# Kernel tuning notes

Hardware: AMD Instinct MI355X
Metric: run time of the kernel (lower is better)

Reference implementation:

```python
import jax, jax.numpy as jnp
import numpy as np

EPS = 1e-5
N_HEAD = 16

def _ln(x, g, b):
    m = jnp.mean(x, -1, keepdims=True)
    v = jnp.mean((x - m) ** 2, -1, keepdims=True)
    return (x - m) * jax.lax.rsqrt(v + EPS) * g + b

def _mlp(x, fc_w, fc_b, proj_w, proj_b):
    h = x @ fc_w.T + fc_b
    h = h * jax.nn.sigmoid(1.702 * h)  # QuickGELU
    return h @ proj_w.T + proj_b

def setup_inputs() -> dict:
    key = jax.random.key(0)
    ks = jax.random.split(key, 16)
    S, B, D, BOX = 577, 8, 1024, 16
    sc = 0.02
    return {
        'x': jax.random.normal(ks[0], (S, B, D), jnp.float32),
        'detection_attn_mask': jax.random.normal(ks[1], (B * BOX * N_HEAD, 1, S), jnp.float32),
        'box_coords': jax.random.uniform(ks[2], (B, BOX, 4), jnp.float32),
        'layers': 24,
        'need_patch': 0,
        'in_proj_w': sc * jax.random.normal(ks[3], (3 * D, D), jnp.float32),
        'in_proj_b': jnp.zeros((3 * D,), jnp.float32),
        'out_w': sc * jax.random.normal(ks[4], (D, D), jnp.float32),
        'out_b': jnp.zeros((D,), jnp.float32),
        'ln1_g': jnp.ones((D,), jnp.float32),
        'ln1_b': jnp.zeros((D,), jnp.float32),
        'ln2_g': jnp.ones((D,), jnp.float32),
        'ln2_b': jnp.zeros((D,), jnp.float32),
        'fc_w': sc * jax.random.normal(ks[5], (4 * D, D), jnp.float32),
        'fc_b': jnp.zeros((4 * D,), jnp.float32),
        'proj_w': sc * jax.random.normal(ks[6], (D, 4 * D), jnp.float32),
        'proj_b': jnp.zeros((D,), jnp.float32),
    }

def reference(x, detection_attn_mask, box_coords, layers, need_patch,
              in_proj_w, in_proj_b, out_w, out_b,
              ln1_g, ln1_b, ln2_g, ln2_b, fc_w, fc_b, proj_w, proj_b):
    # step == layers-1, detection_attn_mask is not None, need_patch is False.
    S, B, D = x.shape
    H = N_HEAD
    hd = D // H
    BOX = box_coords.shape[1]  # uniform boxes per image

    h = _ln(x, ln1_g, ln1_b)                       # [S,B,D]
    qkv = h @ in_proj_w.T + in_proj_b              # [S,B,3D]
    q, k, v = jnp.split(qkv, 3, axis=-1)

    # query is sliced to the CLS token only (q[:, :1, :] after head split)
    q0 = q[0].reshape(B, H, hd) / jnp.sqrt(jnp.asarray(hd, x.dtype))  # [B,H,hd]
    kh = k.reshape(S, B, H, hd).transpose(1, 2, 0, 3)                 # [B,H,S,hd]
    vh = v.reshape(S, B, H, hd).transpose(1, 2, 0, 3)                 # [B,H,S,hd]

    attn = jnp.einsum('bhe,bhse->bhs', q0, kh)     # [B,H,S]

    # mask rows are ordered (batch, box, head); Nt == 1 is squeezed
    mask = detection_attn_mask.reshape(B, BOX, H, S)
    p_exp = jax.nn.softmax(attn[:, None] + mask, axis=-1)             # [B,BOX,H,S]
    out_exp = jnp.einsum('bxhs,bhse->bxhe', p_exp, vh).reshape(B * BOX, D)
    out_exp = out_exp @ out_w.T + out_b            # [B*BOX, D]

    p = jax.nn.softmax(attn, axis=-1)
    out = jnp.einsum('bhs,bhse->bhe', p, vh).reshape(B, D) @ out_w.T + out_b

    cls = x[0] + out                               # residual with CLS token
    cls = cls + _mlp(_ln(cls, ln2_g, ln2_b), fc_w, fc_b, proj_w, proj_b)

    x0_exp = jnp.repeat(x[0], BOX, axis=0)         # [B*BOX, D], batch-major
    mask_cls = x0_exp + out_exp
    mask_cls = mask_cls + _mlp(_ln(mask_cls, ln2_g, ln2_b), fc_w, fc_b, proj_w, proj_b)

    return mask_cls[None], cls[None]               # [1,B*BOX,D], [1,B,D]
```

## Files before the change

### kernel.cpp

```cpp
#include <hip/hip_runtime.h>
#include <stdint.h>

typedef unsigned short u16;
typedef unsigned int u32;
typedef __bf16 bf16x8 __attribute__((ext_vector_type(8)));
typedef float f32x4 __attribute__((ext_vector_type(4)));

__device__ __forceinline__ float bf2f(u16 u) {
  u32 v = ((u32)u) << 16;
  return __builtin_bit_cast(float, v);
}
__device__ __forceinline__ u16 f2bf(float f) {
  u32 u = __builtin_bit_cast(u32, f);
  u32 r = u + 0x7fffu + ((u >> 16) & 1u);
  return (u16)(r >> 16);
}

__device__ __forceinline__ float block_sum4(float v, float* red, int t) {
#pragma unroll
  for (int o = 32; o; o >>= 1) v += __shfl_xor(v, o, 64);
  if ((t & 63) == 0) red[t >> 6] = v;
  __syncthreads();
  float r = red[0] + red[1] + red[2] + red[3];
  __syncthreads();
  return r;
}

#define GLD16(gp, lp)                                                   \
  __builtin_amdgcn_global_load_lds(                                     \
      (const __attribute__((address_space(1))) void*)(gp),              \
      (__attribute__((address_space(3))) void*)(lp), 16, 0, 0)

__global__ __launch_bounds__(256) void cvt_f32_bf16(
    const float* __restrict__ S, u16* __restrict__ D, int n) {
  int i = (blockIdx.x * 256 + threadIdx.x) * 4;
  if (i < n) {
    float4 f = *(const float4*)(S + i);
    u32 lo = (u32)f2bf(f.x) | ((u32)f2bf(f.y) << 16);
    u32 hi = (u32)f2bf(f.z) | ((u32)f2bf(f.w) << 16);
    uint2 val = {lo, hi};
    *(uint2*)(D + i) = val;
  }
}

__global__ __launch_bounds__(256) void ln_rows_f32(
    const float* __restrict__ X, const float* __restrict__ G,
    const float* __restrict__ Bt, u16* __restrict__ O) {
  __shared__ float red[4];
  int row = blockIdx.x, t = threadIdx.x;
  float4 xv = *(const float4*)(X + (size_t)row * 1024 + t * 4);
  float v[4] = {xv.x, xv.y, xv.z, xv.w};
  float s = v[0] + v[1] + v[2] + v[3];
  s = block_sum4(s, red, t);
  float mean = s * (1.f / 1024.f);
  float q = 0.f;
#pragma unroll
  for (int i = 0; i < 4; ++i) { float d = v[i] - mean; q += d * d; }
  q = block_sum4(q, red, t);
  float rstd = rsqrtf(q * (1.f / 1024.f) + 1e-5f);
  float4 g = *(const float4*)(G + t * 4);
  float4 b = *(const float4*)(Bt + t * 4);
  float gg[4] = {g.x, g.y, g.z, g.w}, bb[4] = {b.x, b.y, b.z, b.w};
  u16 o[4];
#pragma unroll
  for (int i = 0; i < 4; ++i) o[i] = f2bf((v[i] - mean) * rstd * gg[i] + bb[i]);
  u32* op = (u32*)(O + (size_t)row * 1024 + t * 4);
  op[0] = (u32)o[0] | ((u32)o[1] << 16);
  op[1] = (u32)o[2] | ((u32)o[3] << 16);
}

__global__ __launch_bounds__(256) void resid_ln_f32(
    const float* __restrict__ X, const float* __restrict__ P,
    const float* __restrict__ G, const float* __restrict__ Bt,
    float* __restrict__ CLS, u16* __restrict__ H2) {
  __shared__ float red[4];
  int row = blockIdx.x, t = threadIdx.x;
  int bi = (row < 128) ? (row >> 4) : (row - 128);
  float4 xv = *(const float4*)(X + (size_t)bi * 1024 + t * 4);
  float4 pv = *(const float4*)(P + (size_t)row * 1024 + t * 4);
  float v[4] = {xv.x + pv.x, xv.y + pv.y, xv.z + pv.z, xv.w + pv.w};
  float* cp = CLS + (size_t)row * 1024 + t * 4;
#pragma unroll
  for (int i = 0; i < 4; ++i) cp[i] = v[i];
  float s = v[0] + v[1] + v[2] + v[3];
  s = block_sum4(s, red, t);
  float mean = s * (1.f / 1024.f);
  float q = 0.f;
#pragma unroll
  for (int i = 0; i < 4; ++i) { float d = v[i] - mean; q += d * d; }
  q = block_sum4(q, red, t);
  float rstd = rsqrtf(q * (1.f / 1024.f) + 1e-5f);
  float4 g = *(const float4*)(G + t * 4);
  float4 b = *(const float4*)(Bt + t * 4);
  float gg[4] = {g.x, g.y, g.z, g.w}, bb[4] = {b.x, b.y, b.z, b.w};
  u16 o[4];
#pragma unroll
  for (int i = 0; i < 4; ++i) o[i] = f2bf((v[i] - mean) * rstd * gg[i] + bb[i]);
  u32* op = (u32*)(H2 + (size_t)row * 1024 + t * 4);
  op[0] = (u32)o[0] | ((u32)o[1] << 16);
  op[1] = (u32)o[2] | ((u32)o[3] << 16);
}

__global__ __launch_bounds__(256) void gemm_bt_128(
    const u16* __restrict__ A, int lda, const u16* __restrict__ W, int ldw,
    const float* __restrict__ bias, u16* __restrict__ C, int ldc,
    int M, int N, int K) {
  __shared__ u16 As[128 * 64];
  __shared__ u16 Bs[128 * 64];
  int t = threadIdx.x, lane = t & 63, wv = t >> 6;
  int bm = blockIdx.x * 128, bn = blockIdx.y * 128;
  int quad = lane >> 4, rlow = lane & 15;
  int lrow = lane >> 3, lcol = (lane & 7) * 8;
  int wrow = (wv & 1) * 64, wcol = (wv >> 1) * 64;
  f32x4 acc[4][4] = {};

  for (int k0 = 0; k0 < K; k0 += 64) {
    __syncthreads();
#pragma unroll
    for (int j = 0; j < 4; ++j) {
      int rb = j * 4 + wv;
      int row = rb * 8 + lrow;
      int gm = bm + row; if (gm >= M) gm = M - 1;
      GLD16(A + (size_t)gm * lda + k0 + lcol, &As[rb * 8 * 64]);
      int gn = bn + row; if (gn >= N) gn = N - 1;
      GLD16(W + (size_t)gn * ldw + k0 + lcol, &Bs[rb * 8 * 64]);
    }
    __syncthreads();
#pragma unroll
    for (int kk = 0; kk < 64; kk += 32) {
      bf16x8 a[4], b[4];
#pragma unroll
      for (int i = 0; i < 4; ++i)
        a[i] = *(const bf16x8*)(&As[(wrow + i * 16 + rlow) * 64 + kk + quad * 8]);
#pragma unroll
      for (int j = 0; j < 4; ++j)
        b[j] = *(const bf16x8*)(&Bs[(wcol + j * 16 + rlow) * 64 + kk + quad * 8]);
#pragma unroll
      for (int i = 0; i < 4; ++i)
#pragma unroll
        for (int j = 0; j < 4; ++j)
          acc[i][j] = __builtin_amdgcn_mfma_f32_16x16x32_bf16(a[i], b[j], acc[i][j], 0, 0, 0);
    }
  }
#pragma unroll
  for (int j = 0; j < 4; ++j) {
    int gn = bn + wcol + j * 16 + rlow;
    float bv = (gn < N) ? bias[gn] : 0.f;
#pragma unroll
    for (int i = 0; i < 4; ++i)
#pragma unroll
      for (int r = 0; r < 4; ++r) {
        int gm = bm + wrow + i * 16 + quad * 4 + r;
        if (gm < M && gn < N) C[(size_t)gm * ldc + gn] = f2bf(acc[i][j][r] + bv);
      }
  }
}

#define LDT 72
__global__ __launch_bounds__(256) void gemm_bt_splitk(
    const u16* __restrict__ A, int lda, const u16* __restrict__ W, int ldw,
    float* __restrict__ ACC, int ldc, int M, int N, int KC) {
  __shared__ u16 As[64 * LDT];
  __shared__ u16 Bs[64 * LDT];
  int t = threadIdx.x;
  int bm = blockIdx.x * 64, bn = blockIdx.y * 64;
  int kbase = blockIdx.z * KC;
  int lane = t & 63, wv = t >> 6;
  f32x4 acc[4] = {};
  int srow = t >> 3;
  int scol = (t & 7) * 8;

  for (int k0 = kbase; k0 < kbase + KC; k0 += 64) {
    __syncthreads();
#pragma unroll
    for (int rr = 0; rr < 2; ++rr) {
      int r = srow + rr * 32;
      int gm = bm + r;
      uint4 da = {0, 0, 0, 0};
      if (gm < M) da = *(const uint4*)(A + (size_t)gm * lda + k0 + scol);
      *(uint4*)(&As[r * LDT + scol]) = da;
      int gn = bn + r;
      uint4 dw = {0, 0, 0, 0};
      if (gn < N) dw = *(const uint4*)(W + (size_t)gn * ldw + k0 + scol);
      *(uint4*)(&Bs[r * LDT + scol]) = dw;
    }
    __syncthreads();
    int quad = lane >> 4, rlow = lane & 15;
#pragma unroll
    for (int kk = 0; kk < 64; kk += 32) {
      bf16x8 a = *(const bf16x8*)(&As[(wv * 16 + rlow) * LDT + kk + quad * 8]);
#pragma unroll
      for (int j = 0; j < 4; ++j) {
        bf16x8 b = *(const bf16x8*)(&Bs[(j * 16 + rlow) * LDT + kk + quad * 8]);
        acc[j] = __builtin_amdgcn_mfma_f32_16x16x32_bf16(a, b, acc[j], 0, 0, 0);
      }
    }
  }
  int quad = lane >> 4, cidx = lane & 15;
#pragma unroll
  for (int j = 0; j < 4; ++j) {
    int gn = bn + j * 16 + cidx;
#pragma unroll
    for (int r = 0; r < 4; ++r) {
      int gm = bm + wv * 16 + quad * 4 + r;
      if (gm < M && gn < N) atomicAdd(&ACC[(size_t)gm * ldc + gn], acc[j][r]);
    }
  }
}

__global__ __launch_bounds__(256) void acc_init(
    float* __restrict__ ACC, const float* __restrict__ bias, int nmask, int total) {
  int i = (blockIdx.x * 256 + threadIdx.x) * 4;
  if (i < total) {
#pragma unroll
    for (int k = 0; k < 4; ++k) ACC[i + k] = bias[(i + k) & nmask];
  }
}

__global__ __launch_bounds__(256) void gelu_cvt(
    const float* __restrict__ ACC, u16* __restrict__ O, int total) {
  int i = (blockIdx.x * 256 + threadIdx.x) * 4;
  if (i < total) {
#pragma unroll
    for (int k = 0; k < 4; ++k) {
      float v = ACC[i + k];
      O[i + k] = f2bf(v / (1.f + __expf(-1.702f * v)));
    }
  }
}

__global__ __launch_bounds__(256) void final_out(
    const float* __restrict__ ACC, const float* __restrict__ CLS,
    float* __restrict__ O, int total) {
  int i = (blockIdx.x * 256 + threadIdx.x) * 4;
  if (i < total) {
#pragma unroll
    for (int k = 0; k < 4; ++k) O[i + k] = ACC[i + k] + CLS[i + k];
  }
}

__global__ __launch_bounds__(256) void qw_build(
    const float* __restrict__ Q0, const float* __restrict__ WK,
    const float* __restrict__ BK, u16* __restrict__ QW, float* __restrict__ C0) {
  int bh = blockIdx.x, b = bh >> 4, h = bh & 15;
  __shared__ float qs[64];
  int t = threadIdx.x;
  if (t < 64) qs[t] = Q0[b * 1024 + h * 64 + t] * 0.125f;
  __syncthreads();
  float acc[4] = {0.f, 0.f, 0.f, 0.f};
  int d0 = t * 4;
#pragma unroll 4
  for (int n = 0; n < 64; ++n) {
    float4 w = *(const float4*)(WK + (size_t)(h * 64 + n) * 1024 + d0);
    float q = qs[n];
    acc[0] += q * w.x;
    acc[1] += q * w.y;
    acc[2] += q * w.z;
    acc[3] += q * w.w;
  }
  u16 o[4];
#pragma unroll
  for (int i = 0; i < 4; ++i) o[i] = f2bf(acc[i]);
  u32* op = (u32*)(QW + (size_t)bh * 1024 + d0);
  op[0] = (u32)o[0] | ((u32)o[1] << 16);
  op[1] = (u32)o[2] | ((u32)o[3] << 16);
  if (t == 0) {
    float c = 0.f;
    for (int n = 0; n < 64; ++n) c += qs[n] * BK[h * 64 + n];
    C0[bh] = c;
  }
}

#define HLD 516
__global__ __launch_bounds__(256) void attn_dot(
    const u16* __restrict__ H, const u16* __restrict__ QW,
    const float* __restrict__ C0, float* __restrict__ ATT) {
  __shared__ u32 Hs[16 * HLD];
  int b = blockIdx.y, s0 = blockIdx.x * 16, t = threadIdx.x;
  for (int idx = t; idx < 16 * 512; idx += 256) {
    int row = idx >> 9, col = idx & 511;
    int s = s0 + row;
    u32 v = 0;
    if (s < 577) v = *(const u32*)(H + ((size_t)(s * 8 + b) << 10) + col * 2);
    Hs[row * HLD + col] = v;
  }
  __syncthreads();
  int si = t & 15, hh = t >> 4;
  int s = s0 + si;
  if (s < 577) {
    const u32* hr = &Hs[si * HLD];
    const u32* qr = (const u32*)(QW + (size_t)(b * 16 + hh) * 1024);
    float acc = 0.f;
    for (int d = 0; d < 512; d += 4) {
      uint4 hv = *(const uint4*)(&hr[d]);
      uint4 qv = *(const uint4*)(&qr[d]);
      acc += bf2f(hv.x & 0xffff) * bf2f(qv.x & 0xffff) + bf2f(hv.x >> 16) * bf2f(qv.x >> 16);
      acc += bf2f(hv.y & 0xffff) * bf2f(qv.y & 0xffff) + bf2f(hv.y >> 16) * bf2f(qv.y >> 16);
      acc += bf2f(hv.z & 0xffff) * bf2f(qv.z & 0xffff) + bf2f(hv.z >> 16) * bf2f(qv.z >> 16);
      acc += bf2f(hv.w & 0xffff) * bf2f(qv.w & 0xffff) + bf2f(hv.w >> 16) * bf2f(qv.w >> 16);
    }
    ATT[(size_t)(b * 16 + hh) * 577 + s] = acc + C0[b * 16 + hh];
  }
}

__global__ __launch_bounds__(256) void softmax_pv(
    const float* __restrict__ ATT, const float* __restrict__ MASK,
    const u16* __restrict__ V, u16* __restrict__ AO) {
  const int S = 577;
  int blk = blockIdx.x;
  int b = blk / 272, rem = blk % 272;
  int x = rem >> 4, h = rem & 15;
  __shared__ float p[S];
  __shared__ float redm[4];
  __shared__ float reds[4];
  __shared__ float partial[256];
  int t = threadIdx.x, lane = t & 63, wv = t >> 6;
  const float* arow = ATT + (size_t)(b * 16 + h) * S;
  float lmax = -3e38f;
  for (int s = t; s < S; s += 256) {
    float v = arow[s];
    if (x < 16) v += MASK[(size_t)((b * 16 + x) * 16 + h) * S + s];
    p[s] = v;
    lmax = fmaxf(lmax, v);
  }
#pragma unroll
  for (int o = 32; o; o >>= 1) lmax = fmaxf(lmax, __shfl_xor(lmax, o, 64));
  if (lane == 0) redm[wv] = lmax;
  __syncthreads();
  float m = fmaxf(fmaxf(redm[0], redm[1]), fmaxf(redm[2], redm[3]));
  float lsum = 0.f;
  for (int s = t; s < S; s += 256) {
    float e = __expf(p[s] - m);
    p[s] = e;
    lsum += e;
  }
#pragma unroll
  for (int o = 32; o; o >>= 1) lsum += __shfl_xor(lsum, o, 64);
  if (lane == 0) reds[wv] = lsum;
  __syncthreads();
  float inv = 1.f / (reds[0] + reds[1] + reds[2] + reds[3]);
  float acc = 0.f;
  const u16* vb = V + h * 64 + lane;
  int s = wv;
  for (; s + 28 < S; s += 32) {
    float w0 = p[s], w1 = p[s + 4], w2 = p[s + 8], w3 = p[s + 12];
    float w4 = p[s + 16], w5 = p[s + 20], w6 = p[s + 24], w7 = p[s + 28];
    float v0 = bf2f(vb[(size_t)((s)*8 + b) << 10]);
    float v1 = bf2f(vb[(size_t)((s + 4) * 8 + b) << 10]);
    float v2 = bf2f(vb[(size_t)((s + 8) * 8 + b) << 10]);
    float v3 = bf2f(vb[(size_t)((s + 12) * 8 + b) << 10]);
    float v4 = bf2f(vb[(size_t)((s + 16) * 8 + b) << 10]);
    float v5 = bf2f(vb[(size_t)((s + 20) * 8 + b) << 10]);
    float v6 = bf2f(vb[(size_t)((s + 24) * 8 + b) << 10]);
    float v7 = bf2f(vb[(size_t)((s + 28) * 8 + b) << 10]);
    acc += w0 * v0 + w1 * v1 + w2 * v2 + w3 * v3;
    acc += w4 * v4 + w5 * v5 + w6 * v6 + w7 * v7;
  }
  for (; s < S; s += 4) acc += p[s] * bf2f(vb[(size_t)(s * 8 + b) << 10]);
  partial[t] = acc;
  __syncthreads();
  if (t < 64) {
    float r = (partial[t] + partial[t + 64] + partial[t + 128] + partial[t + 192]) * inv;
    int row = (x < 16) ? (b * 16 + x) : (128 + b);
    AO[(size_t)row * 1024 + h * 64 + t] = f2bf(r);
  }
}

extern "C" void kernel_launch(void* const* d_in, const int* in_sizes, int n_in,
                              void* d_out, int out_size, void* d_ws, size_t ws_size,
                              hipStream_t stream) {
  const float* x      = (const float*)d_in[0];
  const float* mask   = (const float*)d_in[1];
  const float* in_w   = (const float*)d_in[5];
  const float* in_b   = (const float*)d_in[6];
  const float* out_w  = (const float*)d_in[7];
  const float* out_b  = (const float*)d_in[8];
  const float* ln1_g  = (const float*)d_in[9];
  const float* ln1_b  = (const float*)d_in[10];
  const float* ln2_g  = (const float*)d_in[11];
  const float* ln2_b  = (const float*)d_in[12];
  const float* fc_w   = (const float*)d_in[13];
  const float* fc_b   = (const float*)d_in[14];
  const float* proj_w = (const float*)d_in[15];
  const float* proj_b = (const float*)d_in[16];
  float* out = (float*)d_out;

  const int SB = 577 * 8;
  char* base = (char*)d_ws;
  size_t off = 0;
  auto alloc = [&](size_t bytes) {
    char* p = base + off;
    off += (bytes + 255) & ~(size_t)255;
    return p;
  };
  u16* wqkv_b  = (u16*)alloc((size_t)3072 * 1024 * 2);
  u16* wout_b  = (u16*)alloc((size_t)1024 * 1024 * 2);
  u16* wfc_b   = (u16*)alloc((size_t)4096 * 1024 * 2);
  u16* wproj_b = (u16*)alloc((size_t)4096 * 1024 * 2);
  u16* h        = (u16*)alloc((size_t)SB * 1024 * 2);
  u16* v        = (u16*)alloc((size_t)SB * 1024 * 2);
  float* accQ   = (float*)alloc(8 * 1024 * 4);
  u16* qw       = (u16*)alloc(128 * 1024 * 2);
  float* c0     = (float*)alloc(128 * 4);
  float* attn   = (float*)alloc(128 * 577 * 4);
  u16* attn_out = (u16*)alloc(136 * 1024 * 2);
  float* accO   = (float*)alloc(136 * 1024 * 4);
  float* clspre = (float*)alloc(136 * 1024 * 4);
  u16* h2       = (u16*)alloc(136 * 1024 * 2);
  float* accF   = (float*)alloc((size_t)136 * 4096 * 4);
  u16* hg       = (u16*)alloc((size_t)136 * 4096 * 2);
  float* accP   = (float*)alloc(136 * 1024 * 4);

  cvt_f32_bf16<<<3072, 256, 0, stream>>>(in_w, wqkv_b, 3072 * 1024);
  cvt_f32_bf16<<<1024, 256, 0, stream>>>(out_w, wout_b, 1024 * 1024);
  cvt_f32_bf16<<<4096, 256, 0, stream>>>(fc_w, wfc_b, 4096 * 1024);
  cvt_f32_bf16<<<4096, 256, 0, stream>>>(proj_w, wproj_b, 4096 * 1024);

  ln_rows_f32<<<SB, 256, 0, stream>>>(x, ln1_g, ln1_b, h);
  gemm_bt_128<<<dim3(37, 8), 256, 0, stream>>>(
      h, 1024, wqkv_b + (size_t)2048 * 1024, 1024, in_b + 2048, v, 1024,
      SB, 1024, 1024);
  acc_init<<<8, 256, 0, stream>>>(accQ, in_b, 1023, 8 * 1024);
  gemm_bt_splitk<<<dim3(1, 16, 8), 256, 0, stream>>>(
      h, 1024, wqkv_b, 1024, accQ, 1024, 8, 1024, 128);
  qw_build<<<128, 256, 0, stream>>>(accQ, in_w + (size_t)1024 * 1024,
                                    in_b + 1024, qw, c0);
  attn_dot<<<dim3(37, 8), 256, 0, stream>>>(h, qw, c0, attn);
  softmax_pv<<<8 * 17 * 16, 256, 0, stream>>>(attn, mask, v, attn_out);
  acc_init<<<136, 256, 0, stream>>>(accO, out_b, 1023, 136 * 1024);
  gemm_bt_splitk<<<dim3(3, 16, 8), 256, 0, stream>>>(
      attn_out, 1024, wout_b, 1024, accO, 1024, 136, 1024, 128);
  resid_ln_f32<<<136, 256, 0, stream>>>(x, accO, ln2_g, ln2_b, clspre, h2);
  acc_init<<<544, 256, 0, stream>>>(accF, fc_b, 4095, 136 * 4096);
  gemm_bt_splitk<<<dim3(3, 64, 4), 256, 0, stream>>>(
      h2, 1024, wfc_b, 1024, accF, 4096, 136, 4096, 256);
  gelu_cvt<<<544, 256, 0, stream>>>(accF, hg, 136 * 4096);
  acc_init<<<136, 256, 0, stream>>>(accP, proj_b, 1023, 136 * 1024);
  gemm_bt_splitk<<<dim3(3, 16, 16), 256, 0, stream>>>(
      hg, 4096, wproj_b, 4096, accP, 1024, 136, 1024, 256);
  final_out<<<136, 256, 0, stream>>>(accP, clspre, out, 136 * 1024);

  (void)in_sizes; (void)n_in; (void)out_size; (void)ws_size;
}
```

Measured before the change: 282.6 us.

## Replace split-K atomics with per-slice partial buffers and fused reductions

Each split-K GEMM now writes its partial sums to its own slice buffer with plain stores instead of doing atomicAdd into a bias-initialised accumulator. The slices are summed, with the bias added, inside the consumer kernels (qw_build, residual+LN, GELU, final output), so the acc_init launches go away. The four weight-conversion launches are merged into one segmented kernel, and the unused K-slice of the in-projection weights is no longer converted. The trade-off is more workspace and more bytes read in the reduction kernels, in exchange for no atomic contention and fewer launches.

```diff
diff --git a/kernel.cpp b/kernel.cpp
--- a/kernel.cpp
+++ b/kernel.cpp
@@ -31,16 +31,21 @@
       (const __attribute__((address_space(1))) void*)(gp),              \
       (__attribute__((address_space(3))) void*)(lp), 16, 0, 0)
 
-__global__ __launch_bounds__(256) void cvt_f32_bf16(
-    const float* __restrict__ S, u16* __restrict__ D, int n) {
-  int i = (blockIdx.x * 256 + threadIdx.x) * 4;
-  if (i < n) {
-    float4 f = *(const float4*)(S + i);
-    u32 lo = (u32)f2bf(f.x) | ((u32)f2bf(f.y) << 16);
-    u32 hi = (u32)f2bf(f.z) | ((u32)f2bf(f.w) << 16);
-    uint2 val = {lo, hi};
-    *(uint2*)(D + i) = val;
-  }
+struct CvtSegs {
+  const float* src[5];
+  u16* dst[5];
+  int nblk[6];
+};
+__global__ __launch_bounds__(256) void cvt_all(CvtSegs segs) {
+  int blk = blockIdx.x;
+  int s = 0;
+  while (s < 4 && blk >= segs.nblk[s + 1]) ++s;
+  int i = (blk - segs.nblk[s]) * 1024 + threadIdx.x * 4;
+  float4 f = *(const float4*)(segs.src[s] + i);
+  u32 lo = (u32)f2bf(f.x) | ((u32)f2bf(f.y) << 16);
+  u32 hi = (u32)f2bf(f.z) | ((u32)f2bf(f.w) << 16);
+  uint2 val = {lo, hi};
+  *(uint2*)(segs.dst[s] + i) = val;
 }
 
 __global__ __launch_bounds__(256) void ln_rows_f32(
@@ -69,16 +74,22 @@
   op[1] = (u32)o[2] | ((u32)o[3] << 16);
 }
 
-__global__ __launch_bounds__(256) void resid_ln_f32(
-    const float* __restrict__ X, const float* __restrict__ P,
-    const float* __restrict__ G, const float* __restrict__ Bt,
-    float* __restrict__ CLS, u16* __restrict__ H2) {
+__global__ __launch_bounds__(256) void resid_ln_red(
+    const float* __restrict__ X, const float* __restrict__ OP,
+    const float* __restrict__ OB, const float* __restrict__ G,
+    const float* __restrict__ Bt, float* __restrict__ CLS, u16* __restrict__ H2) {
   __shared__ float red[4];
+  const int PS = 136 * 1024;
   int row = blockIdx.x, t = threadIdx.x;
   int bi = (row < 128) ? (row >> 4) : (row - 128);
   float4 xv = *(const float4*)(X + (size_t)bi * 1024 + t * 4);
-  float4 pv = *(const float4*)(P + (size_t)row * 1024 + t * 4);
-  float v[4] = {xv.x + pv.x, xv.y + pv.y, xv.z + pv.z, xv.w + pv.w};
+  float4 ob = *(const float4*)(OB + t * 4);
+  float v[4] = {xv.x + ob.x, xv.y + ob.y, xv.z + ob.z, xv.w + ob.w};
+#pragma unroll
+  for (int z = 0; z < 8; ++z) {
+    float4 pv = *(const float4*)(OP + (size_t)z * PS + (size_t)row * 1024 + t * 4);
+    v[0] += pv.x; v[1] += pv.y; v[2] += pv.z; v[3] += pv.w;
+  }
   float* cp = CLS + (size_t)row * 1024 + t * 4;
 #pragma unroll
   for (int i = 0; i < 4; ++i) cp[i] = v[i];
@@ -157,14 +168,15 @@
 }
 
 #define LDT 72
-__global__ __launch_bounds__(256) void gemm_bt_splitk(
+__global__ __launch_bounds__(256) void gemm_bt_splitk_p(
     const u16* __restrict__ A, int lda, const u16* __restrict__ W, int ldw,
-    float* __restrict__ ACC, int ldc, int M, int N, int KC) {
+    float* __restrict__ P, int pstride, int ldc, int M, int N, int KC) {
   __shared__ u16 As[64 * LDT];
   __shared__ u16 Bs[64 * LDT];
   int t = threadIdx.x;
   int bm = blockIdx.x * 64, bn = blockIdx.y * 64;
   int kbase = blockIdx.z * KC;
+  float* PZ = P + (size_t)blockIdx.z * pstride;
   int lane = t & 63, wv = t >> 6;
   f32x4 acc[4] = {};
   int srow = t >> 3;
@@ -203,49 +215,60 @@
 #pragma unroll
     for (int r = 0; r < 4; ++r) {
       int gm = bm + wv * 16 + quad * 4 + r;
-      if (gm < M && gn < N) atomicAdd(&ACC[(size_t)gm * ldc + gn], acc[j][r]);
-    }
-  }
-}
-
-__global__ __launch_bounds__(256) void acc_init(
-    float* __restrict__ ACC, const float* __restrict__ bias, int nmask, int total) {
+      if (gm < M && gn < N) PZ[(size_t)gm * ldc + gn] = acc[j][r];
+    }
+  }
+}
+
+__global__ __launch_bounds__(256) void gelu_red(
+    const float* __restrict__ FP, const float* __restrict__ FB,
+    u16* __restrict__ O, int total) {
+  const int PS = 136 * 4096;
   int i = (blockIdx.x * 256 + threadIdx.x) * 4;
   if (i < total) {
 #pragma unroll
-    for (int k = 0; k < 4; ++k) ACC[i + k] = bias[(i + k) & nmask];
-  }
-}
-
-__global__ __launch_bounds__(256) void gelu_cvt(
-    const float* __restrict__ ACC, u16* __restrict__ O, int total) {
+    for (int k = 0; k < 4; ++k) {
+      int idx = i + k;
+      float v = FB[idx & 4095];
+#pragma unroll
+      for (int z = 0; z < 4; ++z) v += FP[(size_t)z * PS + idx];
+      O[idx] = f2bf(v / (1.f + __expf(-1.702f * v)));
+    }
+  }
+}
+
+__global__ __launch_bounds__(256) void final_red(
+    const float* __restrict__ PP, const float* __restrict__ PB,
+    const float* __restrict__ CLS, float* __restrict__ O, int total) {
+  const int PS = 136 * 1024;
   int i = (blockIdx.x * 256 + threadIdx.x) * 4;
   if (i < total) {
 #pragma unroll
     for (int k = 0; k < 4; ++k) {
-      float v = ACC[i + k];
-      O[i + k] = f2bf(v / (1.f + __expf(-1.702f * v)));
-    }
-  }
-}
-
-__global__ __launch_bounds__(256) void final_out(
-    const float* __restrict__ ACC, const float* __restrict__ CLS,
-    float* __restrict__ O, int total) {
-  int i = (blockIdx.x * 256 + threadIdx.x) * 4;
-  if (i < total) {
-#pragma unroll
-    for (int k = 0; k < 4; ++k) O[i + k] = ACC[i + k] + CLS[i + k];
+      int idx = i + k;
+      float v = PB[idx & 1023] + CLS[idx];
+#pragma unroll
+      for (int z = 0; z < 16; ++z) v += PP[(size_t)z * PS + idx];
+      O[idx] = v;
+    }
   }
 }
 
 __global__ __launch_bounds__(256) void qw_build(
-    const float* __restrict__ Q0, const float* __restrict__ WK,
-    const float* __restrict__ BK, u16* __restrict__ QW, float* __restrict__ C0) {
+    const float* __restrict__ QP, const float* __restrict__ QB,
+    const float* __restrict__ WK, const float* __restrict__ BK,
+    u16* __restrict__ QW, float* __restrict__ C0) {
+  const int PS = 8 * 1024;
   int bh = blockIdx.x, b = bh >> 4, h = bh & 15;
   __shared__ float qs[64];
   int t = threadIdx.x;
-  if (t < 64) qs[t] = Q0[b * 1024 + h * 64 + t] * 0.125f;
+  if (t < 64) {
+    int n = h * 64 + t;
+    float q = QB[n];
+#pragma unroll
+    for (int z = 0; z < 8; ++z) q += QP[(size_t)z * PS + b * 1024 + n];
+    qs[t] = q * 0.125f;
+  }
   __syncthreads();
   float acc[4] = {0.f, 0.f, 0.f, 0.f};
   int d0 = t * 4;
@@ -393,52 +416,53 @@
     off += (bytes + 255) & ~(size_t)255;
     return p;
   };
-  u16* wqkv_b  = (u16*)alloc((size_t)3072 * 1024 * 2);
+  u16* wq_b    = (u16*)alloc((size_t)1024 * 1024 * 2);
+  u16* wv_b    = (u16*)alloc((size_t)1024 * 1024 * 2);
   u16* wout_b  = (u16*)alloc((size_t)1024 * 1024 * 2);
   u16* wfc_b   = (u16*)alloc((size_t)4096 * 1024 * 2);
   u16* wproj_b = (u16*)alloc((size_t)4096 * 1024 * 2);
   u16* h        = (u16*)alloc((size_t)SB * 1024 * 2);
   u16* v        = (u16*)alloc((size_t)SB * 1024 * 2);
-  float* accQ   = (float*)alloc(8 * 1024 * 4);
+  float* Qp     = (float*)alloc((size_t)8 * 8 * 1024 * 4);
   u16* qw       = (u16*)alloc(128 * 1024 * 2);
   float* c0     = (float*)alloc(128 * 4);
   float* attn   = (float*)alloc(128 * 577 * 4);
   u16* attn_out = (u16*)alloc(136 * 1024 * 2);
-  float* accO   = (float*)alloc(136 * 1024 * 4);
+  float* Op     = (float*)alloc((size_t)8 * 136 * 1024 * 4);
   float* clspre = (float*)alloc(136 * 1024 * 4);
   u16* h2       = (u16*)alloc(136 * 1024 * 2);
-  float* accF   = (float*)alloc((size_t)136 * 4096 * 4);
+  float* Fp     = (float*)alloc((size_t)4 * 136 * 4096 * 4);
   u16* hg       = (u16*)alloc((size_t)136 * 4096 * 2);
-  float* accP   = (float*)alloc(136 * 1024 * 4);
-
-  cvt_f32_bf16<<<3072, 256, 0, stream>>>(in_w, wqkv_b, 3072 * 1024);
-  cvt_f32_bf16<<<1024, 256, 0, stream>>>(out_w, wout_b, 1024 * 1024);
-  cvt_f32_bf16<<<4096, 256, 0, stream>>>(fc_w, wfc_b, 4096 * 1024);
-  cvt_f32_bf16<<<4096, 256, 0, stream>>>(proj_w, wproj_b, 4096 * 1024);
+  float* Pp     = (float*)alloc((size_t)16 * 136 * 1024 * 4);
+
+  CvtSegs segs;
+  segs.src[0] = in_w;                      segs.dst[0] = wq_b;
+  segs.src[1] = in_w + (size_t)2048*1024;  segs.dst[1] = wv_b;
+  segs.src[2] = out_w;                     segs.dst[2] = wout_b;
+  segs.src[3] = fc_w;                      segs.dst[3] = wfc_b;
+  segs.src[4] = proj_w;                    segs.dst[4] = wproj_b;
+  segs.nblk[0] = 0;    segs.nblk[1] = 1024; segs.nblk[2] = 2048;
+  segs.nblk[3] = 3072; segs.nblk[4] = 7168; segs.nblk[5] = 11264;
+  cvt_all<<<11264, 256, 0, stream>>>(segs);
 
   ln_rows_f32<<<SB, 256, 0, stream>>>(x, ln1_g, ln1_b, h);
   gemm_bt_128<<<dim3(37, 8), 256, 0, stream>>>(
-      h, 1024, wqkv_b + (size_t)2048 * 1024, 1024, in_b + 2048, v, 1024,
-      SB, 1024, 1024);
-  acc_init<<<8, 256, 0, stream>>>(accQ, in_b, 1023, 8 * 1024);
-  gemm_bt_splitk<<<dim3(1, 16, 8), 256, 0, stream>>>(
-      h, 1024, wqkv_b, 1024, accQ, 1024, 8, 1024, 128);
-  qw_build<<<128, 256, 0, stream>>>(accQ, in_w + (size_t)1024 * 1024,
+      h, 1024, wv_b, 1024, in_b + 2048, v, 1024, SB, 1024, 1024);
+  gemm_bt_splitk_p<<<dim3(1, 16, 8), 256, 0, stream>>>(
+      h, 1024, wq_b, 1024, Qp, 8 * 1024, 1024, 8, 1024, 128);
+  qw_build<<<128, 256, 0, stream>>>(Qp, in_b, in_w + (size_t)1024 * 1024,
                                     in_b + 1024, qw, c0);
   attn_dot<<<dim3(37, 8), 256, 0, stream>>>(h, qw, c0, attn);
   softmax_pv<<<8 * 17 * 16, 256, 0, stream>>>(attn, mask, v, attn_out);
-  acc_init<<<136, 256, 0, stream>>>(accO, out_b, 1023, 136 * 1024);
-  gemm_bt_splitk<<<dim3(3, 16, 8), 256, 0, stream>>>(
-      attn_out, 1024, wout_b, 1024, accO, 1024, 136, 1024, 128);
-  resid_ln_f32<<<136, 256, 0, stream>>>(x, accO, ln2_g, ln2_b, clspre, h2);
-  acc_init<<<544, 256, 0, stream>>>(accF, fc_b, 4095, 136 * 4096);
-  gemm_bt_splitk<<<dim3(3, 64, 4), 256, 0, stream>>>(
-      h2, 1024, wfc_b, 1024, accF, 4096, 136, 4096, 256);
-  gelu_cvt<<<544, 256, 0, stream>>>(accF, hg, 136 * 4096);
-  acc_init<<<136, 256, 0, stream>>>(accP, proj_b, 1023, 136 * 1024);
-  gemm_bt_splitk<<<dim3(3, 16, 16), 256, 0, stream>>>(
-      hg, 4096, wproj_b, 4096, accP, 1024, 136, 1024, 256);
-  final_out<<<136, 256, 0, stream>>>(accP, clspre, out, 136 * 1024);
+  gemm_bt_splitk_p<<<dim3(3, 16, 8), 256, 0, stream>>>(
+      attn_out, 1024, wout_b, 1024, Op, 136 * 1024, 1024, 136, 1024, 128);
+  resid_ln_red<<<136, 256, 0, stream>>>(x, Op, out_b, ln2_g, ln2_b, clspre, h2);
+  gemm_bt_splitk_p<<<dim3(3, 64, 4), 256, 0, stream>>>(
+      h2, 1024, wfc_b, 1024, Fp, 136 * 4096, 4096, 136, 4096, 256);
+  gelu_red<<<544, 256, 0, stream>>>(Fp, fc_b, hg, 136 * 4096);
+  gemm_bt_splitk_p<<<dim3(3, 16, 16), 256, 0, stream>>>(
+      hg, 4096, wproj_b, 4096, Pp, 136 * 1024, 1024, 136, 1024, 256);
+  final_red<<<136, 256, 0, stream>>>(Pp, proj_b, clspre, out, 136 * 1024);
 
   (void)in_sizes; (void)n_in; (void)out_size; (void)ws_size;
 }
```

New measurement: 267.6 us. 1.06x faster.
